# Kernel optimization log

Hardware: AMD Instinct MI355X
Metric: run time of the kernel (lower is better)

## Reference

```python
import jax, jax.numpy as jnp
import numpy as np
from jax import lax

EPS = 1e-5

def setup_inputs() -> dict:
    key = jax.random.key(0)
    k1, k2, k3, k4, k5, k6 = jax.random.split(key, 6)
    x = jax.random.normal(k1, (1, 64, 31, 96, 96), dtype=jnp.float32)
    # small init scale keeps gate pre-activations in a sane range
    w = jax.random.normal(k2, (256, 64, 3, 3, 3), dtype=jnp.float32) * 0.05
    gamma = jax.random.uniform(k3, (256,), dtype=jnp.float32)
    beta = jax.random.normal(k4, (256,), dtype=jnp.float32) * 0.1
    mean = jax.random.normal(k5, (256,), dtype=jnp.float32) * 0.1
    var = jax.random.uniform(k6, (256,), dtype=jnp.float32) + 0.5
    return {"x": x, "w": w, "gamma": gamma, "beta": beta, "mean": mean, "var": var}

def _bcast(p):
    return p[None, :, None, None, None]

def reference(x, w, gamma, beta, mean, var):
    # Conv3d (bias=False), stride 1, padding 1, NCDHW
    gates = lax.conv_general_dilated(
        x, w, window_strides=(1, 1, 1), padding=[(1, 1)] * 3,
        dimension_numbers=("NCDHW", "OIDHW", "NCDHW"))
    # BatchNorm3d (inference, running stats)
    scale = gamma * lax.rsqrt(var + EPS)
    gates = gates * _bcast(scale) + _bcast(beta - mean * scale)
    C = 64  # out_channels
    Wx = jnp.tanh(gates[:, 0 * C:1 * C])
    ft = jax.nn.sigmoid(gates[:, 1 * C:2 * C])
    rt = jax.nn.sigmoid(gates[:, 2 * C:3 * C])
    X = jnp.tanh(gates[:, 3 * C:4 * C])  # act == 'tanh'
    # time axis (dim 2) to front: (D, B, C, H, W)
    Wt = jnp.moveaxis(Wx, 2, 0)
    Ft = jnp.moveaxis(ft, 2, 0)
    Rt = jnp.moveaxis(rt, 2, 0)
    Xt = jnp.moveaxis(X, 2, 0)
    # t = 0: Ct = 1 - ft (note: Wx unused at first step, per source)
    C0 = 1.0 - Ft[0]
    h0 = Rt[0] * C0 + (1.0 - Rt[0]) * Xt[0]
    def step(Ct, inp):
        wx, f, r, xx = inp
        Ct = f * Ct + (1.0 - f) * wx
        ht = r * Ct + (1.0 - r) * xx
        return Ct, ht
    _, hs = lax.scan(step, C0, (Wt[1:], Ft[1:], Rt[1:], Xt[1:]))
    hts = jnp.concatenate([h0[None], hs], axis=0)  # (D,B,C,H,W)
    return jnp.moveaxis(hts, 0, 2)  # (B,C,D,H,W)
```

## Files before the change

### kernel.cpp

```cpp
#include <hip/hip_runtime.h>
#include <cstddef>

#define CI_  64
#define CO_  256
#define DD_  31
#define HH_  96
#define WW_  96
#define HW_  (HH_*WW_)
#define DHW_ (DD_*HW_)
#define EPSV 1e-5f

#define PD_   33
#define PH_   98
#define PW_   98
#define PHW_  9604
#define PDHW_ 316932

#define S_COL 8
#define S_CIG 144
#define S_ROW 1152
#define S_DD  11520
#define NTASK 4320
#define NTASKP 4352
#define XH_N  (NTASKP*8)

#define NTILE 72
#define NBLK  (NTILE*DD_)
#define GSP   128

typedef _Float16 half8   __attribute__((ext_vector_type(8)));
typedef _Float16 half4v  __attribute__((ext_vector_type(4)));
typedef float    float4v __attribute__((ext_vector_type(4)));

__device__ __forceinline__ void gl_lds16(const _Float16* g, _Float16* l) {
  __builtin_amdgcn_global_load_lds(
      (const __attribute__((address_space(1))) unsigned int*)(g),
      (__attribute__((address_space(3))) unsigned int*)(l), 16, 0, 0);
}

__global__ __launch_bounds__(256) void repack_w_k(const float* __restrict__ w,
                                                  _Float16* __restrict__ wr2) {
  int idx = blockIdx.x * 256 + threadIdx.x;
  if (idx >= 55296) return;
  int lw   = idx & 15;
  int quad = (idx >> 4) & 3;
  int cog  = (idx >> 6) & 15;
  int tkc  = idx >> 10;
  int kc   = tkc & 1;
  int t    = tkc >> 1;
  int co   = cog * 16 + lw;
  int cib  = kc * 32 + quad * 8;
  half8 v;
#pragma unroll
  for (int s = 0; s < 8; s++)
    v[s] = (_Float16)w[(size_t)co * 1728 + (size_t)(cib + s) * 27 + t];
  *(half8*)(wr2 + (size_t)idx * 8) = v;
}

__global__ __launch_bounds__(256) void pad_zero_k(_Float16* __restrict__ xt) {
  int p = blockIdx.x * 256 + threadIdx.x;
  if (p >= PDHW_) return;
  int pd  = p / PHW_;
  int rem = p - pd * PHW_;
  int ph  = rem / PW_;
  int pw  = rem - ph * PW_;
  bool in = (pd >= 1) & (pd <= DD_) & (ph >= 1) & (ph <= HH_) & (pw >= 1) & (pw <= WW_);
  if (in) return;
  half8 z = (half8)(_Float16)0.f;
#pragma unroll
  for (int cig = 0; cig < 8; cig++)
    *(half8*)(xt + ((size_t)cig * PDHW_ + p) * 8) = z;
}

__global__ __launch_bounds__(256) void transpose_x_k(const float* __restrict__ x,
                                                     _Float16* __restrict__ xt) {
  int idx = blockIdx.x * 256 + threadIdx.x;
  if (idx >= 31 * 96 * 24) return;
  int wq  = idx % 24;
  int rem = idx / 24;
  int h   = rem % 96;
  int d   = rem / 96;
  const float* xp = x + (size_t)d * HW_ + (size_t)h * WW_ + wq * 4;
  size_t p0 = (size_t)(d + 1) * PHW_ + (size_t)(h + 1) * PW_ + (wq * 4 + 1);
#pragma unroll 1
  for (int cig = 0; cig < 8; cig++) {
    float4 vv[8];
#pragma unroll
    for (int s = 0; s < 8; s++)
      vv[s] = *(const float4*)(xp + (size_t)(cig * 8 + s) * DHW_);
#pragma unroll
    for (int k = 0; k < 4; k++) {
      half8 o;
#pragma unroll
      for (int s = 0; s < 8; s++) o[s] = (_Float16)(&vv[s].x)[k];
      *(half8*)(xt + ((size_t)cig * PDHW_ + p0 + k) * 8) = o;
    }
  }
}

__global__ __launch_bounds__(512, 4) void conv_mfma_k(
    const _Float16* __restrict__ xt, const _Float16* __restrict__ wr2,
    const float* __restrict__ gamma, const float* __restrict__ beta,
    const float* __restrict__ mean, const float* __restrict__ var,
    _Float16* __restrict__ gates)
{
  __shared__ _Float16 xh[XH_N];

  const int bid  = blockIdx.x;
  const int flat = (bid & 7) * 279 + (bid >> 3);
  const int d    = flat / NTILE;
  const int bx   = flat - d * NTILE;
  const int wti  = bx % 6;
  const int hti  = bx / 6;
  const int h0   = hti * 8, w0 = wti * 16;

  const int tid  = threadIdx.x;
  const int lane = tid & 63;
  const int wave = __builtin_amdgcn_readfirstlane(tid >> 6);
  const int wm   = wave >> 2;
  const int wn   = wave & 3;
  const int lw   = lane & 15;
  const int quad = lane >> 4;

#pragma unroll 1
  for (int it = 0; it < 9; ++it) {
    const int wb = it * 512 + wave * 64;
    if (wb < NTASKP) {
      const int task = wb + lane;
      const int tt   = task < NTASK ? task : (NTASK - 1);
      int col = tt % 18;
      int rc  = tt / 18;
      int cig = rc & 7;
      int dr  = rc >> 3;
      int dd  = dr / 10;
      int row = dr - dd * 10;
      const _Float16* g = xt + (((size_t)cig * PDHW_ + (size_t)(d + dd) * PHW_ +
                                 (size_t)(h0 + row) * PW_ + (w0 + col)) << 3);
      gl_lds16(g, xh + (size_t)wb * 8);
    }
  }

  float4v acc[4][4];
#pragma unroll
  for (int m = 0; m < 4; m++)
#pragma unroll
    for (int j = 0; j < 4; j++) acc[m][j] = (float4v)0.f;

  __syncthreads();

  const int abase0 = quad * S_CIG + lw * S_COL + (wm * 4) * S_ROW;
#pragma unroll 1
  for (int t9 = 0; t9 < 9; ++t9) {
    const int kd = t9 / 3;
    const int kh = t9 - kd * 3;
#pragma unroll
    for (int kc = 0; kc < 2; ++kc) {
#pragma unroll
      for (int kw = 0; kw < 3; ++kw) {
        const int t = t9 * 3 + kw;
        const _Float16* bp = wr2 + (((size_t)((t * 2 + kc) * 16 + wn * 4)) << 9) + (lane << 3);
        half8 bf[4];
#pragma unroll
        for (int j = 0; j < 4; ++j) bf[j] = *(const half8*)(bp + ((size_t)j << 9));
        const int ab = abase0 + kd * S_DD + kh * S_ROW + (kc * 4) * S_CIG + kw * S_COL;
#pragma unroll
        for (int m = 0; m < 4; ++m) {
          half8 af = *(const half8*)(xh + ab + m * S_ROW);
#pragma unroll
          for (int j = 0; j < 4; ++j)
            acc[m][j] = __builtin_amdgcn_mfma_f32_16x16x32_f16(af, bf[j], acc[m][j], 0, 0, 0);
        }
      }
    }
  }

  _Float16* gb = gates + ((size_t)(d * NTILE + bx) * 256) * GSP;
  const bool istanh = (wn == 0) || (wn == 3);
#pragma unroll
  for (int j = 0; j < 4; j++) {
    const int co = wn * 64 + j * 16 + lw;
    const float s  = gamma[co] * rsqrtf(var[co] + EPSV);
    const float bb = fmaf(-mean[co], s, beta[co]);
#pragma unroll
    for (int m = 0; m < 4; m++) {
      half4v hv;
#pragma unroll
      for (int reg = 0; reg < 4; reg++) {
        float v = fmaf(acc[m][j][reg], s, bb);
        float a;
        if (istanh) {
          float tt = __expf(-2.f * fabsf(v));
          float r  = (1.f - tt) * __builtin_amdgcn_rcpf(1.f + tt);
          a = copysignf(r, v);
        } else {
          a = __builtin_amdgcn_rcpf(1.f + __expf(-v));
        }
        hv[reg] = (_Float16)a;
      }
      *(half4v*)(gb + (size_t)co * GSP + (wm * 4 + m) * 16 + quad * 4) = hv;
    }
  }
}

__global__ __launch_bounds__(256) void recurrence_k(const _Float16* __restrict__ gates,
                                                    float* __restrict__ out) {
  const int idx = blockIdx.x * 256 + threadIdx.x;
  const int q   = idx & 31;
  const int t2  = idx >> 5;
  const int c   = t2 / NTILE;
  const int bx  = t2 - c * NTILE;
  const int hti = bx / 6, wti = bx - hti * 6;
  const int sp  = q * 4;
  const int h   = hti * 8 + (sp >> 4);
  const int w   = wti * 16 + (sp & 15);

  const size_t DSTR = (size_t)NTILE * 256 * GSP;
  const _Float16* g0 = gates + (size_t)bx * 256 * GSP + sp;
  float* op = out + (size_t)c * DHW_ + (size_t)h * WW_ + w;

#define LD(dv, gate) (*(const half4v*)(g0 + (size_t)(dv) * DSTR + (size_t)(c + ((gate) << 6)) * GSP))

  half4v cf = LD(0, 1), cr = LD(0, 2), cx = LD(0, 3);
  half4v nwx = LD(1, 0), nf = LD(1, 1), nr = LD(1, 2), nx = LD(1, 3);
  float C[4];
  {
    float4 st;
#pragma unroll
    for (int k = 0; k < 4; k++) {
      C[k] = 1.f - (float)cf[k];
      float r0 = (float)cr[k], x0 = (float)cx[k];
      (&st.x)[k] = fmaf(r0, C[k] - x0, x0);
    }
    *(float4*)op = st;
  }
#pragma unroll 1
  for (int d = 1; d < DD_; d++) {
    half4v cwx = nwx; cf = nf; cr = nr; cx = nx;
    if (d < DD_ - 1) {
      nwx = LD(d + 1, 0); nf = LD(d + 1, 1);
      nr  = LD(d + 1, 2); nx = LD(d + 1, 3);
    }
    float4 st;
#pragma unroll
    for (int k = 0; k < 4; k++) {
      float wx0 = (float)cwx[k], f0 = (float)cf[k], r0 = (float)cr[k], x0 = (float)cx[k];
      C[k] = fmaf(f0, C[k] - wx0, wx0);
      (&st.x)[k] = fmaf(r0, C[k] - x0, x0);
    }
    *(float4*)(op + (size_t)d * HW_) = st;
  }
#undef LD
}

extern "C" void kernel_launch(void* const* d_in, const int* in_sizes, int n_in,
                              void* d_out, int out_size, void* d_ws, size_t ws_size,
                              hipStream_t stream) {
  const float* x     = (const float*)d_in[0];
  const float* w     = (const float*)d_in[1];
  const float* gamma = (const float*)d_in[2];
  const float* beta  = (const float*)d_in[3];
  const float* mean  = (const float*)d_in[4];
  const float* var   = (const float*)d_in[5];
  float* out = (float*)d_out;

  _Float16* wr2   = (_Float16*)d_ws;
  _Float16* xt    = (_Float16*)((char*)d_ws + 884736);
  _Float16* gates = (_Float16*)((char*)d_ws + 884736 + 40567296);

  repack_w_k<<<216, 256, 0, stream>>>(w, wr2);
  pad_zero_k<<<(PDHW_ + 255) / 256, 256, 0, stream>>>(xt);
  transpose_x_k<<<(31 * 96 * 24 + 255) / 256, 256, 0, stream>>>(x, xt);
  conv_mfma_k<<<NBLK, 512, 0, stream>>>(xt, wr2, gamma, beta, mean, var, gates);
  recurrence_k<<<(64 * NTILE * 32) / 256, 256, 0, stream>>>(gates, out);
}
```

Baseline: 421.9 us.

## Double-buffer conv weight loads with MFMA priority and move activations into recurrence

```diff
diff --git a/kernel.cpp b/kernel.cpp
--- a/kernel.cpp
+++ b/kernel.cpp
@@ -149,33 +149,56 @@
   __syncthreads();
 
   const int abase0 = quad * S_CIG + lw * S_COL + (wm * 4) * S_ROW;
-#pragma unroll 1
-  for (int t9 = 0; t9 < 9; ++t9) {
-    const int kd = t9 / 3;
-    const int kh = t9 - kd * 3;
-#pragma unroll
-    for (int kc = 0; kc < 2; ++kc) {
-#pragma unroll
-      for (int kw = 0; kw < 3; ++kw) {
-        const int t = t9 * 3 + kw;
-        const _Float16* bp = wr2 + (((size_t)((t * 2 + kc) * 16 + wn * 4)) << 9) + (lane << 3);
-        half8 bf[4];
-#pragma unroll
-        for (int j = 0; j < 4; ++j) bf[j] = *(const half8*)(bp + ((size_t)j << 9));
-        const int ab = abase0 + kd * S_DD + kh * S_ROW + (kc * 4) * S_CIG + kw * S_COL;
-#pragma unroll
-        for (int m = 0; m < 4; ++m) {
-          half8 af = *(const half8*)(xh + ab + m * S_ROW);
-#pragma unroll
-          for (int j = 0; j < 4; ++j)
-            acc[m][j] = __builtin_amdgcn_mfma_f32_16x16x32_f16(af, bf[j], acc[m][j], 0, 0, 0);
-        }
-      }
-    }
-  }
+
+#define LOADB(bf, s)                                                          \
+  {                                                                           \
+    const int t9_ = (s) / 6, sub_ = (s) - 6 * t9_;                            \
+    const int kc_ = sub_ / 3, kw_ = sub_ - 3 * kc_;                           \
+    const int t_  = t9_ * 3 + kw_;                                            \
+    const _Float16* bp_ =                                                     \
+        wr2 + (((size_t)((t_ * 2 + kc_) * 16 + wn * 4)) << 9) + (lane << 3);  \
+    bf[0] = *(const half8*)(bp_);                                             \
+    bf[1] = *(const half8*)(bp_ + (1 << 9));                                  \
+    bf[2] = *(const half8*)(bp_ + (2 << 9));                                  \
+    bf[3] = *(const half8*)(bp_ + (3 << 9));                                  \
+  }
+
+#define STEP(s, bf)                                                           \
+  {                                                                           \
+    const int t9_ = (s) / 6, sub_ = (s) - 6 * t9_;                            \
+    const int kc_ = sub_ / 3, kw_ = sub_ - 3 * kc_;                           \
+    const int kd_ = t9_ / 3, kh_ = t9_ - 3 * kd_;                             \
+    const int ab_ = abase0 + kd_ * S_DD + kh_ * S_ROW + kc_ * (4 * S_CIG) +   \
+                    kw_ * S_COL;                                              \
+    half8 af0 = *(const half8*)(xh + ab_);                                    \
+    half8 af1 = *(const half8*)(xh + ab_ + S_ROW);                            \
+    half8 af2 = *(const half8*)(xh + ab_ + 2 * S_ROW);                        \
+    half8 af3 = *(const half8*)(xh + ab_ + 3 * S_ROW);                        \
+    __builtin_amdgcn_s_setprio(1);                                            \
+    _Pragma("unroll")                                                         \
+    for (int j = 0; j < 4; ++j) {                                             \
+      acc[0][j] = __builtin_amdgcn_mfma_f32_16x16x32_f16(af0, bf[j], acc[0][j], 0, 0, 0); \
+      acc[1][j] = __builtin_amdgcn_mfma_f32_16x16x32_f16(af1, bf[j], acc[1][j], 0, 0, 0); \
+      acc[2][j] = __builtin_amdgcn_mfma_f32_16x16x32_f16(af2, bf[j], acc[2][j], 0, 0, 0); \
+      acc[3][j] = __builtin_amdgcn_mfma_f32_16x16x32_f16(af3, bf[j], acc[3][j], 0, 0, 0); \
+    }                                                                         \
+    __builtin_amdgcn_s_setprio(0);                                            \
+  }
+
+  half8 bfa[4], bfb[4];
+  LOADB(bfa, 0)
+#pragma unroll 1
+  for (int i = 0; i < 27; ++i) {
+    const int s0 = 2 * i;
+    LOADB(bfb, s0 + 1)
+    STEP(s0, bfa)
+    if (i < 26) LOADB(bfa, s0 + 2)
+    STEP(s0 + 1, bfb)
+  }
+#undef LOADB
+#undef STEP
 
   _Float16* gb = gates + ((size_t)(d * NTILE + bx) * 256) * GSP;
-  const bool istanh = (wn == 0) || (wn == 3);
 #pragma unroll
   for (int j = 0; j < 4; j++) {
     const int co = wn * 64 + j * 16 + lw;
@@ -185,21 +208,19 @@
     for (int m = 0; m < 4; m++) {
       half4v hv;
 #pragma unroll
-      for (int reg = 0; reg < 4; reg++) {
-        float v = fmaf(acc[m][j][reg], s, bb);
-        float a;
-        if (istanh) {
-          float tt = __expf(-2.f * fabsf(v));
-          float r  = (1.f - tt) * __builtin_amdgcn_rcpf(1.f + tt);
-          a = copysignf(r, v);
-        } else {
-          a = __builtin_amdgcn_rcpf(1.f + __expf(-v));
-        }
-        hv[reg] = (_Float16)a;
-      }
+      for (int reg = 0; reg < 4; reg++)
+        hv[reg] = (_Float16)fmaf(acc[m][j][reg], s, bb);
       *(half4v*)(gb + (size_t)co * GSP + (wm * 4 + m) * 16 + quad * 4) = hv;
     }
   }
+}
+
+__device__ __forceinline__ float tanh_f(float v) {
+  float t = __expf(-2.f * fabsf(v));
+  return copysignf((1.f - t) * __builtin_amdgcn_rcpf(1.f + t), v);
+}
+__device__ __forceinline__ float sigm_f(float v) {
+  return __builtin_amdgcn_rcpf(1.f + __expf(-v));
 }
 
 __global__ __launch_bounds__(256) void recurrence_k(const _Float16* __restrict__ gates,
@@ -227,8 +248,8 @@
     float4 st;
 #pragma unroll
     for (int k = 0; k < 4; k++) {
-      C[k] = 1.f - (float)cf[k];
-      float r0 = (float)cr[k], x0 = (float)cx[k];
+      C[k] = 1.f - sigm_f((float)cf[k]);
+      float r0 = sigm_f((float)cr[k]), x0 = tanh_f((float)cx[k]);
       (&st.x)[k] = fmaf(r0, C[k] - x0, x0);
     }
     *(float4*)op = st;
@@ -243,7 +264,10 @@
     float4 st;
 #pragma unroll
     for (int k = 0; k < 4; k++) {
-      float wx0 = (float)cwx[k], f0 = (float)cf[k], r0 = (float)cr[k], x0 = (float)cx[k];
+      float wx0 = tanh_f((float)cwx[k]);
+      float f0  = sigm_f((float)cf[k]);
+      float r0  = sigm_f((float)cr[k]);
+      float x0  = tanh_f((float)cx[k]);
       C[k] = fmaf(f0, C[k] - wx0, wx0);
       (&st.x)[k] = fmaf(r0, C[k] - x0, x0);
     }
```

New measurement: 421.5 us. Within noise of the previous version (-0.1%).
